# Kernel tuning notes

Measured on AMD Instinct MI355X. Metric: run time of the kernel, lower is better.

## Reference

```python
import jax, jax.numpy as jnp
import numpy as np


def setup_inputs() -> dict:
    key = jax.random.key(0)
    k1, k2 = jax.random.split(key)
    B, S, D, O = 4, 4096, 2048, 2048
    inputs = jax.random.normal(k1, (B, S, D), dtype=jnp.float32)
    # truncated-normal-like init with stddev 1/sqrt(fan_in)
    w = jax.random.normal(k2, (D, O), dtype=jnp.float32) * (1.0 / np.sqrt(D))
    b = jnp.zeros((O,), dtype=jnp.float32)
    return {"inputs": inputs, "w": w, "b": b}


def reference(inputs, w, b):
    # logsumexp-semiring linear layer (basis=None path):
    #   out = log(exp(inputs - max_in) @ exp(w - max_w)) + max_in + max_w + b
    max_inputs = jnp.max(inputs)          # global scalar max for stabilization
    max_w = jnp.max(w)
    exp_inputs = jnp.exp(inputs - max_inputs)   # [B, S, D]
    exp_w = jnp.exp(w - max_w)                  # [D, O]
    out = jnp.log(jnp.dot(exp_inputs, exp_w))   # [B, S, O]
    out = out + (max_inputs + max_w)
    out = out + b                               # broadcast bias over [B, S, O]
    return out
```

## Files before the change

kernel.cpp:

```cpp
#include <hip/hip_runtime.h>

typedef int   i32x4v __attribute__((ext_vector_type(4)));
typedef int   i32x8v __attribute__((ext_vector_type(8)));
typedef float f32x16 __attribute__((ext_vector_type(16)));

#define GLOBAL_AS(p) ((const __attribute__((address_space(1))) void*)(p))
#define LDS_AS(p)    ((__attribute__((address_space(3))) void*)(p))
#define BAR()     __builtin_amdgcn_s_barrier()
#define VMCNT(n)  asm volatile("s_waitcnt vmcnt(" #n ")" ::: "memory")

__device__ inline int fp4_code(float v) {
  return (v > 0.25f) + (v > 0.75f) + (v > 1.25f) + (v > 1.75f) +
         (v > 2.5f) + (v > 3.5f) + (v > 5.0f);
}

__global__ void expcvt_a4_kernel(const float* __restrict__ x,
                                 unsigned char* __restrict__ A4,
                                 unsigned char* __restrict__ SAt,
                                 int M, int K) {
  const int NKB = K >> 5;
  const int t = blockIdx.x * blockDim.x + threadIdx.x;
  const int m = t / NKB, kb = t - m * NKB;
  if (m >= M) return;
  const float4* xs4 = (const float4*)(x + (size_t)m * K + kb * 32);
  float a[32];
  float bm = -3.0e38f;
#pragma unroll
  for (int j = 0; j < 8; ++j) {
    float4 v = xs4[j];
    a[4 * j] = v.x; a[4 * j + 1] = v.y; a[4 * j + 2] = v.z; a[4 * j + 3] = v.w;
    bm = fmaxf(bm, fmaxf(fmaxf(v.x, v.y), fmaxf(v.z, v.w)));
  }
  int e = (int)ceilf(bm * 1.44269504f - 2.58496250f);
  e = min(127, max(-126, e));
  SAt[(size_t)kb * M + m] = (unsigned char)(e + 127);
  uint4 u;
  unsigned d[4];
#pragma unroll
  for (int g = 0; g < 4; ++g) {
    unsigned acc = 0;
#pragma unroll
    for (int j = 0; j < 8; ++j) {
      float v = exp2f(a[g * 8 + j] * 1.44269504f - (float)e);
      acc |= (unsigned)fp4_code(v) << (4 * j);
    }
    d[g] = acc;
  }
  u.x = d[0]; u.y = d[1]; u.z = d[2]; u.w = d[3];
  *(uint4*)(A4 + (size_t)m * (K >> 1) + kb * 16) = u;
}

__global__ void expcvt_wt4_kernel(const float* __restrict__ w,
                                  unsigned char* __restrict__ Bt4,
                                  unsigned char* __restrict__ SBt,
                                  int D, int O) {
  __shared__ float tile[32][33];
  int c0 = blockIdx.x * 32;
  int r0 = blockIdx.y * 32;
  int tx = threadIdx.x;
  int ty = threadIdx.y;
#pragma unroll
  for (int j = 0; j < 4; ++j) {
    int r = r0 + ty + j * 8;
    tile[ty + j * 8][tx] = __expf(w[(size_t)r * O + c0 + tx]);
  }
  __syncthreads();
  if (ty == 0) {
    const int n = tx;
    float bm = 0.0f;
#pragma unroll
    for (int d = 0; d < 32; ++d) bm = fmaxf(bm, tile[d][n]);
    int e = (int)ceilf(__log2f(bm) - 2.58496250f);
    e = min(127, max(-126, e));
    SBt[(size_t)(r0 >> 5) * O + c0 + n] = (unsigned char)(e + 127);
    const float inv = exp2f(-(float)e);
    uint4 u;
    unsigned d4[4];
#pragma unroll
    for (int g = 0; g < 4; ++g) {
      unsigned acc = 0;
#pragma unroll
      for (int j = 0; j < 8; ++j)
        acc |= (unsigned)fp4_code(tile[g * 8 + j][n] * inv) << (4 * j);
      d4[g] = acc;
    }
    u.x = d4[0]; u.y = d4[1]; u.z = d4[2]; u.w = d4[3];
    *(uint4*)(Bt4 + (size_t)(c0 + n) * (D >> 1) + (r0 >> 1)) = u;
  }
}


#define MFMA4(MB, NB)                                                        \
  acc[MB][NB] = __builtin_amdgcn_mfma_scale_f32_32x32x64_f8f6f4(             \
      a8[MB], b8[NB], acc[MB][NB], 4, 4, 0, sA[MB], 0, sB[NB]);

__global__ __launch_bounds__(256, 2) void gemm_mx4_kernel(
    const unsigned char* __restrict__ A4, const unsigned char* __restrict__ Bt4,
    const unsigned char* __restrict__ SAt, const unsigned char* __restrict__ SBt,
    const float* __restrict__ bias, float* __restrict__ out,
    int M, int N, int K) {
  __shared__ char lds[39936];

  const int tid = threadIdx.x;
  const int wid = tid >> 6, lane = tid & 63;
  const int l31 = lane & 31, lk = lane >> 5;
  const int NTK = K >> 6;
  const size_t Kb = (size_t)K >> 1;

  const int cpx = gridDim.x >> 3;
  const int v   = (blockIdx.x & 7) * cpx + (blockIdx.x >> 3);
  const int nbn = N >> 8;
  const int bm  = v / nbn, bn = v % nbn;
  const int brow = bm << 7, bcol = bn << 8;

  const int sbl = ((l31 >> 2) ^ (l31 >> 4)) & 1;
  const int c0x = ((lk ^ sbl) << 4);

  const char* gA;
  {
    const int o = tid * 16, row = o >> 5;
    const int sbr = ((row >> 2) ^ (row >> 4)) & 1;
    gA = (const char*)A4 + (size_t)(brow + row) * Kb + ((o & 31) ^ (sbr << 4));
  }
  const char* gB[2];
#pragma unroll
  for (int i = 0; i < 2; ++i) {
    const int o = i * 4096 + tid * 16, row = o >> 5;
    const int sbr = ((row >> 2) ^ (row >> 4)) & 1;
    gB[i] = (const char*)Bt4 + (size_t)(bcol + row) * Kb + ((o & 31) ^ (sbr << 4));
  }
  const char* gS;
  size_t sstep;
  int sdst;
  if (wid == 1)      { gS = (const char*)SBt + bcol + lane * 4;            sstep = 2 * (size_t)N; sdst = 12544; }
  else if (wid == 2) { gS = (const char*)SBt + N + bcol + lane * 4;        sstep = 2 * (size_t)N; sdst = 12800; }
  else {
    gS = (const char*)SAt + ((lane >> 5) ? (size_t)M : 0) + brow + (lane & 31) * 4;
    sstep = 2 * (size_t)M;
    sdst = (wid == 0) ? 12288 : 13056;
  }

  auto STAGE = [&](int t, int s) {
    const int tt = (t < NTK) ? t : NTK - 1;
    char* base = lds + s * 13312;
    __builtin_amdgcn_global_load_lds(GLOBAL_AS(gA + tt * 32),
        LDS_AS(base + tid * 16), 16, 0, 0);
#pragma unroll
    for (int i = 0; i < 2; ++i)
      __builtin_amdgcn_global_load_lds(GLOBAL_AS(gB[i] + tt * 32),
          LDS_AS(base + 4096 + i * 4096 + tid * 16), 16, 0, 0);
    __builtin_amdgcn_global_load_lds(GLOBAL_AS(gS + (size_t)tt * sstep),
        LDS_AS(base + sdst + lane * 4), 4, 0, 0);
  };

  f32x16 acc[4][2];
#pragma unroll
  for (int m = 0; m < 4; ++m)
#pragma unroll
    for (int n = 0; n < 2; ++n) acc[m][n] = (f32x16)0.0f;

  STAGE(0, 0);
  STAGE(1, 1);
  VMCNT(4);
  BAR();

  int s0 = 0, s1 = 1, s2 = 2;
  for (int t = 0; t < NTK; ++t) {
    STAGE(t + 2, s2);

    const char* bufb = lds + s0 * 13312;
    i32x8v a8[4], b8[2];
    int sA[4], sB[2];
#pragma unroll
    for (int mb = 0; mb < 4; ++mb) {
      i32x4v f = *(const i32x4v*)(bufb + mb * 1024 + l31 * 32 + c0x);
      a8[mb] = __builtin_shufflevector(f, f, 0, 1, 2, 3, -1, -1, -1, -1);
      sA[mb] = *(const unsigned char*)(bufb + 12288 + lk * 128 + mb * 32 + l31);
    }
#pragma unroll
    for (int nb = 0; nb < 2; ++nb) {
      i32x4v f = *(const i32x4v*)(bufb + 4096 + wid * 2048 + nb * 1024 +
                                  l31 * 32 + c0x);
      b8[nb] = __builtin_shufflevector(f, f, 0, 1, 2, 3, -1, -1, -1, -1);
      sB[nb] = *(const unsigned char*)(bufb + 12544 + lk * 256 + wid * 64 +
                                       nb * 32 + l31);
    }
    MFMA4(0, 0) MFMA4(1, 0) MFMA4(2, 0) MFMA4(3, 0)
    MFMA4(0, 1) MFMA4(1, 1) MFMA4(2, 1) MFMA4(3, 1)

    VMCNT(4);
    BAR();
    const int sw = s0; s0 = s1; s1 = s2; s2 = sw;
  }

  const int col0 = bcol + wid * 64 + l31;
  const int row0 = brow + lk * 4;
  const float bv0 = bias[col0], bv1 = bias[col0 + 32];
#pragma unroll
  for (int mb = 0; mb < 4; ++mb) {
#pragma unroll
    for (int rg = 0; rg < 16; ++rg) {
      const int row = row0 + mb * 32 + (rg & 3) + 8 * (rg >> 2);
      const size_t ro = (size_t)row * N + col0;
      __builtin_nontemporal_store(__logf(acc[mb][0][rg]) + bv0, &out[ro]);
      __builtin_nontemporal_store(__logf(acc[mb][1][rg]) + bv1, &out[ro + 32]);
    }
  }
}

extern "C" void kernel_launch(void* const* d_in, const int* in_sizes, int n_in,
                              void* d_out, int out_size, void* d_ws, size_t ws_size,
                              hipStream_t stream) {
  const float* inputs = (const float*)d_in[0];
  const float* w      = (const float*)d_in[1];
  const float* bias   = (const float*)d_in[2];
  float* out = (float*)d_out;

  const int O = in_sizes[2];
  const int D = in_sizes[1] / O;
  const size_t MD = (size_t)in_sizes[0];
  const int M = (int)(MD / (size_t)D);

  unsigned char* ws  = (unsigned char*)d_ws;
  unsigned char* A4  = ws;
  unsigned char* Bt4 = ws + MD / 2;
  unsigned char* SAt = Bt4 + (size_t)O * D / 2;
  unsigned char* SBt = SAt + MD / 32;

  const int nthr = (int)((MD / 32 + 255) / 256);
  expcvt_a4_kernel<<<nthr, 256, 0, stream>>>(inputs, A4, SAt, M, D);

  dim3 tg(O / 32, D / 32);
  expcvt_wt4_kernel<<<tg, dim3(32, 8), 0, stream>>>(w, Bt4, SBt, D, O);

  dim3 grid((M / 128) * (O / 256));
  gemm_mx4_kernel<<<grid, 256, 0, stream>>>(A4, Bt4, SAt, SBt, bias, out,
                                            M, O, D);
}
```

Before: 105.8 us.

## Double K-tile depth per stage and pack scale bytes for word-wide LDS reads

The GEMM now loads 128 K-elements per pipeline stage instead of 64, halving the number of barrier/wait iterations and doubling LDS to about 78KB, with a new XOR swizzle for 64-byte rows. The scale producers write A and B scales in an interleaved order so each lane reads its four A scales as one int and B scales as an int2, replacing several byte LDS reads per step. The larger LDS footprint may limit occupancy to two blocks per CU (matching launch bounds), and the swizzle and scale-index math add correctness risk.

```diff
diff --git a/kernel.cpp b/kernel.cpp
--- a/kernel.cpp
+++ b/kernel.cpp
@@ -33,7 +33,8 @@
   }
   int e = (int)ceilf(bm * 1.44269504f - 2.58496250f);
   e = min(127, max(-126, e));
-  SAt[(size_t)kb * M + m] = (unsigned char)(e + 127);
+  SAt[(size_t)kb * M + ((m >> 7) << 7) + ((m & 31) << 2) + ((m >> 5) & 3)] =
+      (unsigned char)(e + 127);
   uint4 u;
   unsigned d[4];
 #pragma unroll
@@ -66,13 +67,14 @@
   }
   __syncthreads();
   if (ty == 0) {
-    const int n = tx;
+    const int n = c0 + tx;
     float bm = 0.0f;
 #pragma unroll
-    for (int d = 0; d < 32; ++d) bm = fmaxf(bm, tile[d][n]);
+    for (int d = 0; d < 32; ++d) bm = fmaxf(bm, tile[d][tx]);
     int e = (int)ceilf(__log2f(bm) - 2.58496250f);
     e = min(127, max(-126, e));
-    SBt[(size_t)(r0 >> 5) * O + c0 + n] = (unsigned char)(e + 127);
+    SBt[(size_t)(r0 >> 5) * O + ((n >> 8) << 8) + ((n & 31) << 3) +
+        ((n >> 5) & 7)] = (unsigned char)(e + 127);
     const float inv = exp2f(-(float)e);
     uint4 u;
     unsigned d4[4];
@@ -81,30 +83,30 @@
       unsigned acc = 0;
 #pragma unroll
       for (int j = 0; j < 8; ++j)
-        acc |= (unsigned)fp4_code(tile[g * 8 + j][n] * inv) << (4 * j);
+        acc |= (unsigned)fp4_code(tile[g * 8 + j][tx] * inv) << (4 * j);
       d4[g] = acc;
     }
     u.x = d4[0]; u.y = d4[1]; u.z = d4[2]; u.w = d4[3];
-    *(uint4*)(Bt4 + (size_t)(c0 + n) * (D >> 1) + (r0 >> 1)) = u;
-  }
-}
-
-
-#define MFMA4(MB, NB)                                                        \
+    *(uint4*)(Bt4 + (size_t)n * (D >> 1) + (r0 >> 1)) = u;
+  }
+}
+
+
+#define MFMA4(MB, NB, AV, BV, SAv, SBv)                                      \
   acc[MB][NB] = __builtin_amdgcn_mfma_scale_f32_32x32x64_f8f6f4(             \
-      a8[MB], b8[NB], acc[MB][NB], 4, 4, 0, sA[MB], 0, sB[NB]);
-
-__global__ __launch_bounds__(256, 2) void gemm_mx4_kernel(
+      AV, BV, acc[MB][NB], 4, 4, 0, SAv, 0, SBv);
+
+__global__ __launch_bounds__(256, 2) void gemm_mx4b_kernel(
     const unsigned char* __restrict__ A4, const unsigned char* __restrict__ Bt4,
     const unsigned char* __restrict__ SAt, const unsigned char* __restrict__ SBt,
     const float* __restrict__ bias, float* __restrict__ out,
     int M, int N, int K) {
-  __shared__ char lds[39936];
+  __shared__ char lds[79872];
 
   const int tid = threadIdx.x;
   const int wid = tid >> 6, lane = tid & 63;
   const int l31 = lane & 31, lk = lane >> 5;
-  const int NTK = K >> 6;
+  const int NTK = K >> 7;
   const size_t Kb = (size_t)K >> 1;
 
   const int cpx = gridDim.x >> 3;
@@ -113,44 +115,63 @@
   const int bm  = v / nbn, bn = v % nbn;
   const int brow = bm << 7, bcol = bn << 8;
 
-  const int sbl = ((l31 >> 2) ^ (l31 >> 4)) & 1;
-  const int c0x = ((lk ^ sbl) << 4);
-
-  const char* gA;
-  {
-    const int o = tid * 16, row = o >> 5;
-    const int sbr = ((row >> 2) ^ (row >> 4)) & 1;
-    gA = (const char*)A4 + (size_t)(brow + row) * Kb + ((o & 31) ^ (sbr << 4));
-  }
-  const char* gB[2];
+  const int swz = ((l31 & 6) << 3) ^ (l31 & 16);
+  const int cR0 = (lk << 5) ^ swz;
+
+  const char* gA[2];
+  const char* gB[4];
 #pragma unroll
   for (int i = 0; i < 2; ++i) {
-    const int o = i * 4096 + tid * 16, row = o >> 5;
-    const int sbr = ((row >> 2) ^ (row >> 4)) & 1;
-    gB[i] = (const char*)Bt4 + (size_t)(bcol + row) * Kb + ((o & 31) ^ (sbr << 4));
-  }
-  const char* gS;
-  size_t sstep;
-  int sdst;
-  if (wid == 1)      { gS = (const char*)SBt + bcol + lane * 4;            sstep = 2 * (size_t)N; sdst = 12544; }
-  else if (wid == 2) { gS = (const char*)SBt + N + bcol + lane * 4;        sstep = 2 * (size_t)N; sdst = 12800; }
-  else {
-    gS = (const char*)SAt + ((lane >> 5) ? (size_t)M : 0) + brow + (lane & 31) * 4;
-    sstep = 2 * (size_t)M;
-    sdst = (wid == 0) ? 12288 : 13056;
-  }
-
-  auto STAGE = [&](int t, int s) {
+    const int o = i * 4096 + tid * 16, row = o >> 6;
+    const int sg = (((row & 6) << 3) ^ (row & 16)) >> 4;
+    const int gl = ((o >> 4) & 3) ^ sg;
+    const int gs = ((gl & 1) << 1) | (gl >> 1);
+    gA[i] = (const char*)A4 + (size_t)(brow + row) * Kb + (gs << 4) + (o & 15);
+  }
+#pragma unroll
+  for (int i = 0; i < 4; ++i) {
+    const int o = i * 4096 + tid * 16, row = o >> 6;
+    const int sg = (((row & 6) << 3) ^ (row & 16)) >> 4;
+    const int gl = ((o >> 4) & 3) ^ sg;
+    const int gs = ((gl & 1) << 1) | (gl >> 1);
+    gB[i] = (const char*)Bt4 + (size_t)(bcol + row) * Kb + (gs << 4) + (o & 15);
+  }
+  const char* gSA = (const char*)SAt + (size_t)lk * M + brow + l31 * 4;
+  const char* gSB = (const char*)SBt + bcol + (lane >> 1) * 8 + (lane & 1) * 4;
+
+  auto STAGE = [&](int t, char* base) {
     const int tt = (t < NTK) ? t : NTK - 1;
-    char* base = lds + s * 13312;
-    __builtin_amdgcn_global_load_lds(GLOBAL_AS(gA + tt * 32),
-        LDS_AS(base + tid * 16), 16, 0, 0);
+    const int koff = tt << 6;
 #pragma unroll
     for (int i = 0; i < 2; ++i)
-      __builtin_amdgcn_global_load_lds(GLOBAL_AS(gB[i] + tt * 32),
-          LDS_AS(base + 4096 + i * 4096 + tid * 16), 16, 0, 0);
-    __builtin_amdgcn_global_load_lds(GLOBAL_AS(gS + (size_t)tt * sstep),
-        LDS_AS(base + sdst + lane * 4), 4, 0, 0);
+      __builtin_amdgcn_global_load_lds(GLOBAL_AS(gA[i] + koff),
+          LDS_AS(base + i * 4096 + wid * 1024), 16, 0, 0);
+#pragma unroll
+    for (int i = 0; i < 4; ++i)
+      __builtin_amdgcn_global_load_lds(GLOBAL_AS(gB[i] + koff),
+          LDS_AS(base + 8192 + i * 4096 + wid * 1024), 16, 0, 0);
+    const size_t t4 = (size_t)(tt << 2);
+    if (wid == 0) {
+      __builtin_amdgcn_global_load_lds(GLOBAL_AS(gSA + t4 * M),
+          LDS_AS(base + 24576), 4, 0, 0);
+      __builtin_amdgcn_global_load_lds(GLOBAL_AS(gSA + t4 * M),
+          LDS_AS(base + 26112), 4, 0, 0);
+    } else if (wid == 1) {
+      __builtin_amdgcn_global_load_lds(GLOBAL_AS(gSA + (t4 + 2) * M),
+          LDS_AS(base + 24832), 4, 0, 0);
+      __builtin_amdgcn_global_load_lds(GLOBAL_AS(gSA + (t4 + 2) * M),
+          LDS_AS(base + 26368), 4, 0, 0);
+    } else if (wid == 2) {
+      __builtin_amdgcn_global_load_lds(GLOBAL_AS(gSB + t4 * N),
+          LDS_AS(base + 25088), 4, 0, 0);
+      __builtin_amdgcn_global_load_lds(GLOBAL_AS(gSB + (t4 + 1) * N),
+          LDS_AS(base + 25344), 4, 0, 0);
+    } else {
+      __builtin_amdgcn_global_load_lds(GLOBAL_AS(gSB + (t4 + 2) * N),
+          LDS_AS(base + 25600), 4, 0, 0);
+      __builtin_amdgcn_global_load_lds(GLOBAL_AS(gSB + (t4 + 3) * N),
+          LDS_AS(base + 25856), 4, 0, 0);
+    }
   };
 
   f32x16 acc[4][2];
@@ -159,39 +180,56 @@
 #pragma unroll
     for (int n = 0; n < 2; ++n) acc[m][n] = (f32x16)0.0f;
 
-  STAGE(0, 0);
-  STAGE(1, 1);
-  VMCNT(4);
+  char* L0 = lds;
+  char* L1 = lds + 26624;
+  char* L2 = lds + 53248;
+
+  STAGE(0, L0);
+  STAGE(1, L1);
+  VMCNT(8);
   BAR();
 
-  int s0 = 0, s1 = 1, s2 = 2;
+  const int shB = (wid & 1) << 4;
+
   for (int t = 0; t < NTK; ++t) {
-    STAGE(t + 2, s2);
-
-    const char* bufb = lds + s0 * 13312;
-    i32x8v a8[4], b8[2];
-    int sA[4], sB[2];
-#pragma unroll
-    for (int mb = 0; mb < 4; ++mb) {
-      i32x4v f = *(const i32x4v*)(bufb + mb * 1024 + l31 * 32 + c0x);
-      a8[mb] = __builtin_shufflevector(f, f, 0, 1, 2, 3, -1, -1, -1, -1);
-      sA[mb] = *(const unsigned char*)(bufb + 12288 + lk * 128 + mb * 32 + l31);
-    }
-#pragma unroll
-    for (int nb = 0; nb < 2; ++nb) {
-      i32x4v f = *(const i32x4v*)(bufb + 4096 + wid * 2048 + nb * 1024 +
-                                  l31 * 32 + c0x);
-      b8[nb] = __builtin_shufflevector(f, f, 0, 1, 2, 3, -1, -1, -1, -1);
-      sB[nb] = *(const unsigned char*)(bufb + 12544 + lk * 256 + wid * 64 +
-                                       nb * 32 + l31);
-    }
-    MFMA4(0, 0) MFMA4(1, 0) MFMA4(2, 0) MFMA4(3, 0)
-    MFMA4(0, 1) MFMA4(1, 1) MFMA4(2, 1) MFMA4(3, 1)
-
-    VMCNT(4);
+    STAGE(t + 2, L2);
+
+    const char* bA = L0;
+    const char* bB = L0 + 8192;
+#pragma unroll
+    for (int h = 0; h < 2; ++h) {
+      const int ch = cR0 ^ (h << 4);
+      i32x8v a8[4], b8[2];
+#pragma unroll
+      for (int mb = 0; mb < 4; ++mb) {
+        i32x4v f = *(const i32x4v*)(bA + (mb * 32 + l31) * 64 + ch);
+        a8[mb] = __builtin_shufflevector(f, f, 0, 1, 2, 3, -1, -1, -1, -1);
+      }
+#pragma unroll
+      for (int nb = 0; nb < 2; ++nb) {
+        i32x4v f = *(const i32x4v*)(bB + (wid * 64 + nb * 32 + l31) * 64 + ch);
+        b8[nb] = __builtin_shufflevector(f, f, 0, 1, 2, 3, -1, -1, -1, -1);
+      }
+      const int kb2 = 2 * h + lk;
+      const int sAw = *(const int*)(L0 + 24576 + (kb2 * 32 + l31) * 4);
+      const int2 sBd = *(const int2*)(L0 + 25088 + kb2 * 256 + l31 * 8);
+      const int sel = (wid < 2) ? sBd.x : sBd.y;
+      const int sB0 = (sel >> shB) & 0xFF;
+      const int sB1 = (sel >> (shB + 8)) & 0xFF;
+      const int sA0 = sAw & 0xFF, sA1 = (sAw >> 8) & 0xFF;
+      const int sA2 = (sAw >> 16) & 0xFF, sA3 = (sAw >> 24) & 0xFF;
+      MFMA4(0, 0, a8[0], b8[0], sA0, sB0) MFMA4(1, 0, a8[1], b8[0], sA1, sB0)
+      MFMA4(2, 0, a8[2], b8[0], sA2, sB0) MFMA4(3, 0, a8[3], b8[0], sA3, sB0)
+      MFMA4(0, 1, a8[0], b8[1], sA0, sB1) MFMA4(1, 1, a8[1], b8[1], sA1, sB1)
+      MFMA4(2, 1, a8[2], b8[1], sA2, sB1) MFMA4(3, 1, a8[3], b8[1], sA3, sB1)
+    }
+
+    VMCNT(8);
     BAR();
-    const int sw = s0; s0 = s1; s1 = s2; s2 = sw;
-  }
+    char* sw = L0; L0 = L1; L1 = L2; L2 = sw;
+  }
+
+  VMCNT(0);
 
   const int col0 = bcol + wid * 64 + l31;
   const int row0 = brow + lk * 4;
@@ -234,6 +272,6 @@
   expcvt_wt4_kernel<<<tg, dim3(32, 8), 0, stream>>>(w, Bt4, SBt, D, O);
 
   dim3 grid((M / 128) * (O / 256));
-  gemm_mx4_kernel<<<grid, 256, 0, stream>>>(A4, Bt4, SAt, SBt, bias, out,
-                                            M, O, D);
-}
+  gemm_mx4b_kernel<<<grid, 256, 0, stream>>>(A4, Bt4, SAt, SBt, bias, out,
+                                             M, O, D);
+}
```

New measurement: 103.5 us. 1.02x faster.
